# Optimization experiments

Hardware: AMD Instinct MI355X
Metric: run time of the kernel (lower is better)

The kernel has to match this reference:

```python
import jax, jax.numpy as jnp
import numpy as np

P, S, IMG = 8, 4, 256          # patch_size, stride, img_size
HID, GH, B = 64, 128, 4        # conv hidden ch, gcn hidden ch, batch
Ph = (IMG - P) // S + 1        # 63 patches per side
N = Ph * Ph                    # 3969 patch-nodes


def _conv(x, w, b):
    y = jax.lax.conv_general_dilated(x, w, (1, 1), 'SAME',
                                     dimension_numbers=('NCHW', 'OIHW', 'NCHW'))
    return y + b[None, :, None, None]


def _img2patch(x):
    # x: [B,1,H,W] -> [B, N, P*P] (row-major patch pixels, matching torch reshape)
    pt = jax.lax.conv_general_dilated_patches(x, (P, P), (S, S), 'VALID')  # [B, P*P, Ph, Pw]
    b = x.shape[0]
    return pt.reshape(b, P * P, N).transpose(0, 2, 1)


def _patch2img(y):
    # y: [b, N, P*P] -> [b, 1, IMG, IMG] via overlap scatter-add
    b = y.shape[0]
    y = y.reshape(b, Ph, Ph, P, P)
    x = jnp.zeros((b, 1, IMG, IMG), y.dtype)
    hi = S * (Ph - 1) + 1
    for i in range(P):          # fixed small loop over patch pixels (64 iters)
        for j in range(P):
            x = x.at[:, 0, i:i + hi:S, j:j + hi:S].add(y[:, :, :, i, j])
    return x


def _gcn(x, adj, w, bias):
    # x: [B,N,F_in], adj: [B,N,N] -> [B,N,F_out]
    support = jnp.einsum('bnf,fg->bng', x, w)
    return jnp.einsum('bnm,bmg->bng', adj, support) + bias


def setup_inputs() -> dict:
    key = jax.random.key(0)
    ks = jax.random.split(key, 14)
    sc = 0.05
    return {
        'input_data': jax.random.normal(ks[0], (B, 1, IMG, IMG), jnp.float32),
        'proj': jax.random.normal(ks[1], (B, 1, IMG, IMG), jnp.float32),
        'adj': jax.random.uniform(ks[2], (B, N, N), jnp.float32) / N,
        'lam': jnp.float32(0.5),
        'conv_w1': jax.random.normal(ks[3], (HID, 1, 3, 3), jnp.float32) * sc,
        'conv_b1': jnp.zeros((HID,), jnp.float32),
        'conv_w2': jax.random.normal(ks[4], (HID, HID, 3, 3), jnp.float32) * sc,
        'conv_b2': jnp.zeros((HID,), jnp.float32),
        'conv_w3': jax.random.normal(ks[5], (1, HID, 3, 3), jnp.float32) * sc,
        'conv_b3': jnp.zeros((1,), jnp.float32),
        'gcn_w3': jax.random.normal(ks[6], (P * P, GH), jnp.float32) * sc,
        'gcn_b3': jnp.zeros((GH,), jnp.float32),
        'gcn_w4': jax.random.normal(ks[7], (GH, P * P), jnp.float32) * sc,
        'gcn_b4': jnp.zeros((P * P,), jnp.float32),
    }


def reference(input_data, proj, adj, lam,
              conv_w1, conv_b1, conv_w2, conv_b2, conv_w3, conv_b3,
              gcn_w3, gcn_b3, gcn_w4, gcn_b4):
    # block1: data-fidelity step (fidelity_module modeled as DC update)
    tmp1 = input_data + lam * (proj - input_data)
    # block2: 3-layer CNN
    h = jax.nn.relu(_conv(input_data, conv_w1, conv_b1))
    h = jax.nn.relu(_conv(h, conv_w2, conv_b2))
    tmp2 = _conv(h, conv_w3, conv_b3)
    # block3/4: patch-graph GCN branch
    patch = _img2patch(input_data)                 # [B, N, P*P]
    g = jax.nn.relu(_gcn(patch, adj, gcn_w3, gcn_b3))
    g = _gcn(g, adj, gcn_w4, gcn_b4)               # [B, N, P*P]
    # Patch2Im with overlap-count normalization mask
    mask = _patch2img(jnp.ones((1, N, P * P), jnp.float32))
    tmp3 = _patch2img(g) / mask
    return jax.nn.relu(tmp1 + tmp2 + tmp3)
```

## Files before the change

kernel.cpp:

```cpp
#include <hip/hip_runtime.h>

#define IMG   256
#define NPIX  65536
#define PH    63
#define NNODE 3969
#define SN    4000
#define HID   64
#define GH    128
#define BATCH 4

typedef __attribute__((ext_vector_type(8))) short short8;
typedef __attribute__((ext_vector_type(4))) float float4v;
typedef unsigned short ushort_t;

__device__ inline ushort_t f2bf(float f) {
    union { float f; unsigned u; } v; v.f = f;
    unsigned r = v.u + 0x7FFF + ((v.u >> 16) & 1);
    return (ushort_t)(r >> 16);
}

__global__ __launch_bounds__(256) void k_cvt_adj(const float* __restrict__ adj,
                                                 ushort_t* __restrict__ adjb) {
    int n = blockIdx.x, b = blockIdx.y;
    const float* src = adj + (size_t)(b * NNODE + n) * NNODE;
    unsigned* dst = (unsigned*)(adjb + (size_t)(b * NNODE + n) * SN);
    for (int c2 = threadIdx.x; c2 < SN / 2; c2 += 256) {
        int c = c2 * 2;
        float f0 = (c < NNODE) ? src[c] : 0.f;
        float f1 = (c + 1 < NNODE) ? src[c + 1] : 0.f;
        dst[c2] = (unsigned)f2bf(f0) | ((unsigned)f2bf(f1) << 16);
    }
}

__global__ __launch_bounds__(256) void k_sup1(const float* __restrict__ in,
                                              const float* __restrict__ w3,
                                              ushort_t* __restrict__ sup1T) {
    int b = blockIdx.z;
    int g = blockIdx.y * 8 + (threadIdx.x >> 5);
    int n = blockIdx.x * 32 + (threadIdx.x & 31);
    ushort_t* dst = sup1T + (size_t)b * GH * SN + (size_t)g * SN + n;
    if (n >= NNODE) { *dst = 0; return; }
    int py = n / PH, px = n - py * PH;
    const float* base = in + (size_t)b * NPIX + (py * 4) * IMG + px * 4;
    float acc = 0.f;
#pragma unroll
    for (int i = 0; i < 8; ++i) {
        float4v v0 = *(const float4v*)&base[i * IMG];
        float4v v1 = *(const float4v*)&base[i * IMG + 4];
        const float* wrow = w3 + (i * 8) * GH + g;
#pragma unroll
        for (int j = 0; j < 4; ++j) acc += v0[j] * wrow[j * GH];
#pragma unroll
        for (int j = 0; j < 4; ++j) acc += v1[j] * wrow[(4 + j) * GH];
    }
    *dst = f2bf(acc);
}

template <int G>
__global__ __launch_bounds__(256) void k_gemm_mfma(const ushort_t* __restrict__ adjb,
                                                   const ushort_t* __restrict__ supT,
                                                   float* __restrict__ C) {
    constexpr int FN = (G == 128) ? 4 : 2;
    const int b = blockIdx.z, ks = blockIdx.y;
    const int node0 = blockIdx.x * 128;
    const int t = threadIdx.x;
    const int lane = t & 63, w = t >> 6;
    const int l15 = lane & 15, q = lane >> 4;
    const int wm0 = (G == 128) ? (w & 1) * 64 : 0;
    const int wn0 = (G == 128) ? (w >> 1) * 64 : w * 32;

    __shared__ ushort_t Als[G][72];
    __shared__ ushort_t Bls[128][72];

    const int k0c = ks * 512;
    const int kend = (k0c + 512 < NNODE) ? (k0c + 512) : NNODE;
    const int kiters = (kend - k0c + 31) >> 5;
    const int npairs = (kiters + 1) >> 1;

    const ushort_t* Ab = supT + (size_t)b * G * SN;
    const ushort_t* Bb = adjb + (size_t)b * NNODE * SN;
    float* Cb = C + (size_t)b * G * SN;

    float4v acc[4][FN];
#pragma unroll
    for (int i = 0; i < 4; ++i)
#pragma unroll
        for (int j = 0; j < FN; ++j)
#pragma unroll
            for (int r = 0; r < 4; ++r) acc[i][j][r] = 0.f;

    for (int kp = 0; kp < npairs; ++kp) {
        const int kb0 = k0c + kp * 64;
        const bool has2 = (kp * 2 + 1 < kiters);
#pragma unroll
        for (int i = 0; i < G / 64; ++i) {
            int idx = t + i * 256;
            int r = idx >> 2, s = idx & 3;
            *(uint4*)&Als[r][s * 8] =
                *(const uint4*)&Ab[(size_t)r * SN + kb0 + s * 8];
        }
#pragma unroll
        for (int i = 0; i < 2; ++i) {
            int idx = t + i * 256;
            int r = idx >> 2, s = idx & 3;
            *(uint4*)&Bls[r][s * 8] =
                *(const uint4*)&Bb[(size_t)(node0 + r) * SN + kb0 + s * 8];
        }
        if (has2) {
#pragma unroll
            for (int i = 0; i < G / 64; ++i) {
                int idx = t + i * 256;
                int r = idx >> 2, s = idx & 3;
                *(uint4*)&Als[r][32 + s * 8] =
                    *(const uint4*)&Ab[(size_t)r * SN + kb0 + 32 + s * 8];
            }
#pragma unroll
            for (int i = 0; i < 2; ++i) {
                int idx = t + i * 256;
                int r = idx >> 2, s = idx & 3;
                *(uint4*)&Bls[r][32 + s * 8] =
                    *(const uint4*)&Bb[(size_t)(node0 + r) * SN + kb0 + 32 + s * 8];
            }
        }
        __syncthreads();
        {
            short8 af[4], bf[FN];
#pragma unroll
            for (int i = 0; i < 4; ++i)
                af[i] = *(const short8*)&Als[wm0 + i * 16 + l15][q * 8];
#pragma unroll
            for (int j = 0; j < FN; ++j)
                bf[j] = *(const short8*)&Bls[wn0 + j * 16 + l15][q * 8];
#pragma unroll
            for (int i = 0; i < 4; ++i)
#pragma unroll
                for (int j = 0; j < FN; ++j)
                    acc[i][j] = __builtin_amdgcn_mfma_f32_16x16x32_bf16(
                        af[i], bf[j], acc[i][j], 0, 0, 0);
        }
        if (has2) {
            short8 af[4], bf[FN];
#pragma unroll
            for (int i = 0; i < 4; ++i)
                af[i] = *(const short8*)&Als[wm0 + i * 16 + l15][32 + q * 8];
#pragma unroll
            for (int j = 0; j < FN; ++j)
                bf[j] = *(const short8*)&Bls[wn0 + j * 16 + l15][32 + q * 8];
#pragma unroll
            for (int i = 0; i < 4; ++i)
#pragma unroll
                for (int j = 0; j < FN; ++j)
                    acc[i][j] = __builtin_amdgcn_mfma_f32_16x16x32_bf16(
                        af[i], bf[j], acc[i][j], 0, 0, 0);
        }
        __syncthreads();
    }
#pragma unroll
    for (int i = 0; i < 4; ++i) {
        int gg = wm0 + i * 16 + q * 4;
#pragma unroll
        for (int j = 0; j < FN; ++j) {
            int nn = node0 + wn0 + j * 16 + l15;
            if (nn < NNODE) {
#pragma unroll
                for (int r = 0; r < 4; ++r)
                    unsafeAtomicAdd(&Cb[(size_t)(gg + r) * SN + nn], acc[i][j][r]);
            }
        }
    }
}

__global__ __launch_bounds__(256) void k_sup2(const float* __restrict__ g1T,
                                              const float* __restrict__ gb3,
                                              const float* __restrict__ w4,
                                              ushort_t* __restrict__ sup2T) {
    int b = blockIdx.z;
    int g = blockIdx.y * 8 + (threadIdx.x >> 5);
    int n = blockIdx.x * 32 + (threadIdx.x & 31);
    const float* gb = g1T + (size_t)b * GH * SN + n;
    float acc = 0.f;
#pragma unroll 8
    for (int k = 0; k < GH; ++k) {
        float v = fmaxf(gb[(size_t)k * SN] + gb3[k], 0.f);
        acc += v * w4[k * 64 + g];
    }
    sup2T[(size_t)b * 64 * SN + (size_t)g * SN + n] = (n < NNODE) ? f2bf(acc) : 0;
}

__global__ __launch_bounds__(256) void k_prepack(const float* __restrict__ w,
                                                 ushort_t* __restrict__ W2p) {
    int idx = blockIdx.x * 256 + threadIdx.x;
    if (idx >= 36864) return;
    int tap = idx >> 12, rem = idx & 4095;
    int oc = rem >> 6, ic = rem & 63;
    W2p[idx] = f2bf(w[(oc * 64 + ic) * 9 + tap]);
}

__global__ __launch_bounds__(256) void k_conv2f(const float* __restrict__ in,
                                                const float* __restrict__ w1,
                                                const float* __restrict__ b1,
                                                const ushort_t* __restrict__ W2p,
                                                const float* __restrict__ b2,
                                                const float* __restrict__ w3c,
                                                float* __restrict__ U) {
    __shared__ ushort_t Xs[340 * 72];
    __shared__ float pre[1088];
    const int b = blockIdx.z;
    const float* inb = in + (size_t)b * NPIX;
    float* Uball = U + (size_t)b * 9 * NPIX;
    const int t = threadIdx.x;
    const int lane = t & 63, w = t >> 6;
    const int l15 = lane & 15, q = lane >> 4;
    const int x0 = blockIdx.x * 32, y0 = blockIdx.y * 8;

    float* sI  = pre;
    float* ws1 = pre + 432;
    float* bs1 = pre + 1008;

    for (int idx = t; idx < 432; idx += 256) {
        int yy = idx / 36, xx = idx - yy * 36;
        int gy = y0 + yy - 2, gx = x0 + xx - 2;
        sI[idx] = (gy >= 0 && gy < IMG && gx >= 0 && gx < IMG) ? inb[gy * IMG + gx] : 0.f;
    }
    for (int idx = t; idx < 576; idx += 256) ws1[idx] = w1[idx];
    if (t < 64) bs1[t] = b1[t];
    __syncthreads();

    for (int idx = t; idx < 2720; idx += 256) {
        int hp = idx >> 3, s = idx & 7;
        int hy = hp / 34, hx = hp - hy * 34;
        int gy = y0 + hy - 1, gx = x0 + hx - 1;
        unsigned pk[4] = {0u, 0u, 0u, 0u};
        if (gy >= 0 && gy < IMG && gx >= 0 && gx < IMG) {
            float r[9];
#pragma unroll
            for (int dy = 0; dy < 3; ++dy)
#pragma unroll
                for (int dx = 0; dx < 3; ++dx)
                    r[dy * 3 + dx] = sI[(hy + dy) * 36 + hx + dx];
#pragma unroll
            for (int h = 0; h < 4; ++h) {
                int oc0 = s * 8 + h * 2;
                float a0 = bs1[oc0], a1 = bs1[oc0 + 1];
#pragma unroll
                for (int k = 0; k < 9; ++k) {
                    a0 += r[k] * ws1[oc0 * 9 + k];
                    a1 += r[k] * ws1[(oc0 + 1) * 9 + k];
                }
                a0 = fmaxf(a0, 0.f); a1 = fmaxf(a1, 0.f);
                pk[h] = (unsigned)f2bf(a0) | ((unsigned)f2bf(a1) << 16);
            }
        }
        *(uint4*)&Xs[hp * 72 + s * 8] = *(uint4*)pk;
    }
    __syncthreads();

    for (int idx = t; idx < 576; idx += 256) pre[idx] = w3c[idx];

    const int wn0 = w * 64;
    int pbase[4];
#pragma unroll
    for (int j = 0; j < 4; ++j) {
        int p = wn0 + j * 16 + l15;
        pbase[j] = (p >> 5) * 34 + (p & 31);
    }

    float4v acc[4][4];
#pragma unroll
    for (int i = 0; i < 4; ++i)
#pragma unroll
        for (int j = 0; j < 4; ++j)
#pragma unroll
            for (int r = 0; r < 4; ++r) acc[i][j][r] = 0.f;

    for (int tap = 0; tap < 9; ++tap) {
        int ky = tap / 3, kx = tap - ky * 3;
        const ushort_t* wp = W2p + tap * 4096;
#pragma unroll
        for (int c = 0; c < 2; ++c) {
            short8 af[4], bf[4];
#pragma unroll
            for (int i = 0; i < 4; ++i)
                af[i] = *(const short8*)&wp[(i * 16 + l15) * 64 + c * 32 + q * 8];
#pragma unroll
            for (int j = 0; j < 4; ++j)
                bf[j] = *(const short8*)&Xs[(pbase[j] + ky * 34 + kx) * 72 + c * 32 + q * 8];
#pragma unroll
            for (int i = 0; i < 4; ++i)
#pragma unroll
                for (int j = 0; j < 4; ++j)
                    acc[i][j] = __builtin_amdgcn_mfma_f32_16x16x32_bf16(
                        af[i], bf[j], acc[i][j], 0, 0, 0);
        }
    }
    __syncthreads();

    float b2r[16];
#pragma unroll
    for (int i = 0; i < 4; ++i)
#pragma unroll
        for (int r = 0; r < 4; ++r) b2r[i * 4 + r] = b2[i * 16 + q * 4 + r];

#pragma unroll
    for (int j = 0; j < 4; ++j) {
        float u[9];
#pragma unroll
        for (int d = 0; d < 9; ++d) u[d] = 0.f;
#pragma unroll
        for (int i = 0; i < 4; ++i)
#pragma unroll
            for (int r = 0; r < 4; ++r) {
                int oc = i * 16 + q * 4 + r;
                float h = fmaxf(acc[i][j][r] + b2r[i * 4 + r], 0.f);
#pragma unroll
                for (int d = 0; d < 9; ++d) u[d] += h * pre[oc * 9 + d];
            }
#pragma unroll
        for (int d = 0; d < 9; ++d) {
            u[d] += __shfl_xor(u[d], 16, 64);
            u[d] += __shfl_xor(u[d], 32, 64);
        }
        int p = wn0 + j * 16 + l15;
        int y = y0 + (p >> 5), x = x0 + (p & 31);
#pragma unroll
        for (int dd = 0; dd < 3; ++dd) {
            int d = q + dd * 4;
            if (d < 9)
                Uball[(size_t)d * NPIX + (size_t)y * IMG + x] = u[d];
        }
    }
}

__global__ __launch_bounds__(256) void k_combine(const float* __restrict__ in,
                                                 const float* __restrict__ proj,
                                                 const float* __restrict__ lamp,
                                                 const float* __restrict__ U,
                                                 const float* __restrict__ bc,
                                                 const float* __restrict__ g2T,
                                                 const float* __restrict__ gb4,
                                                 float* __restrict__ out) {
    int b = blockIdx.z;
    const float* inb = in + (size_t)b * NPIX;
    const float* prb = proj + (size_t)b * NPIX;
    const float* Ub = U + (size_t)b * 9 * NPIX;
    const float* g2b = g2T + (size_t)b * 64 * SN;
    int tx = threadIdx.x & 15, ty = threadIdx.x >> 4;
    int x = blockIdx.x * 16 + tx, y = blockIdx.y * 16 + ty;

    float acc = bc[0];
#pragma unroll
    for (int dy = 0; dy < 3; ++dy) {
        int yy = y + dy - 1;
#pragma unroll
        for (int dx = 0; dx < 3; ++dx) {
            int xx = x + dx - 1;
            if (yy >= 0 && yy < IMG && xx >= 0 && xx < IMG)
                acc += Ub[(size_t)(dy * 3 + dx) * NPIX + (size_t)yy * IMG + xx];
        }
    }

    float iv = inb[y * IMG + x], pv = prb[y * IMG + x];
    float tmp1 = iv + lamp[0] * (pv - iv);

    int pylo = (y >= 4) ? ((y - 4) >> 2) : 0;
    int pyhi = min(62, y >> 2);
    int pxlo = (x >= 4) ? ((x - 4) >> 2) : 0;
    int pxhi = min(62, x >> 2);
    float sum = 0.f;
    int cnt = 0;
    for (int py = pylo; py <= pyhi; ++py)
        for (int px = pxlo; px <= pxhi; ++px) {
            int pix = (y - 4 * py) * 8 + (x - 4 * px);
            sum += g2b[(size_t)pix * SN + (py * PH + px)] + gb4[pix];
            ++cnt;
        }
    float tmp3 = sum / (float)cnt;

    out[(size_t)b * NPIX + y * IMG + x] = fmaxf(tmp1 + acc + tmp3, 0.f);
}

extern "C" void kernel_launch(void* const* d_in, const int* in_sizes, int n_in,
                              void* d_out, int out_size, void* d_ws, size_t ws_size,
                              hipStream_t stream) {
    const float* input = (const float*)d_in[0];
    const float* proj  = (const float*)d_in[1];
    const float* adj   = (const float*)d_in[2];
    const float* lam   = (const float*)d_in[3];
    const float* cw1   = (const float*)d_in[4];
    const float* cb1   = (const float*)d_in[5];
    const float* cw2   = (const float*)d_in[6];
    const float* cb2   = (const float*)d_in[7];
    const float* cw3   = (const float*)d_in[8];
    const float* cb3   = (const float*)d_in[9];
    const float* gw3   = (const float*)d_in[10];
    const float* gb3   = (const float*)d_in[11];
    const float* gw4   = (const float*)d_in[12];
    const float* gb4   = (const float*)d_in[13];
    float* out = (float*)d_out;

    char* base = (char*)d_ws;
    float*    g2T   = (float*)base;
    char*     pool  = base + 4096000;
    ushort_t* adjb  = (ushort_t*)pool;
    ushort_t* sup1T = (ushort_t*)(pool + 127008000);
    float*    g1T   = (float*)(pool + 127008000 + 4096000);
    ushort_t* sup2T = (ushort_t*)(pool + 127008000 + 4096000 + 8192000);
    float*    U     = (float*)pool;
    ushort_t* W2p   = (ushort_t*)(pool + 9437184);

    dim3 blk(256);

    hipMemsetAsync(g1T, 0, 8192000, stream);
    hipMemsetAsync(g2T, 0, 4096000, stream);

    k_cvt_adj<<<dim3(NNODE, BATCH), blk, 0, stream>>>(adj, adjb);
    k_sup1<<<dim3(125, 16, BATCH), blk, 0, stream>>>(input, gw3, sup1T);
    k_gemm_mfma<128><<<dim3(32, 8, BATCH), blk, 0, stream>>>(adjb, sup1T, g1T);
    k_sup2<<<dim3(125, 8, BATCH), blk, 0, stream>>>(g1T, gb3, gw4, sup2T);
    k_gemm_mfma<64><<<dim3(32, 8, BATCH), blk, 0, stream>>>(adjb, sup2T, g2T);

    k_prepack<<<dim3(144), blk, 0, stream>>>(cw2, W2p);
    k_conv2f<<<dim3(8, 32, BATCH), blk, 0, stream>>>(input, cw1, cb1, W2p, cb2, cw3, U);
    k_combine<<<dim3(16, 16, BATCH), blk, 0, stream>>>(
        input, proj, lam, U, cb3, g2T, gb4, out);
}
```

Measured before the change: 694.9 us.

## Replace split-K atomic accumulation with partial buffers and a reduction kernel

The two adjacency GEMMs now split K into 4 chunks instead of 8. Each chunk writes plain stores into its own partial buffer rather than atomically adding into a zeroed output. A small float4 reduction kernel then sums the four partials, and the two memsets are removed. This removes atomic traffic and memset launches but adds extra kernel launches and extra write/read traffic for the partial buffers, and halves the grid's parallelism.

```diff
diff --git a/kernel.cpp b/kernel.cpp
--- a/kernel.cpp
+++ b/kernel.cpp
@@ -59,7 +59,7 @@
 template <int G>
 __global__ __launch_bounds__(256) void k_gemm_mfma(const ushort_t* __restrict__ adjb,
                                                    const ushort_t* __restrict__ supT,
-                                                   float* __restrict__ C) {
+                                                   float* __restrict__ Cp) {
     constexpr int FN = (G == 128) ? 4 : 2;
     const int b = blockIdx.z, ks = blockIdx.y;
     const int node0 = blockIdx.x * 128;
@@ -72,14 +72,14 @@
     __shared__ ushort_t Als[G][72];
     __shared__ ushort_t Bls[128][72];
 
-    const int k0c = ks * 512;
-    const int kend = (k0c + 512 < NNODE) ? (k0c + 512) : NNODE;
+    const int k0c = ks * 992;
+    const int kend = (ks == 3) ? NNODE : k0c + 992;
     const int kiters = (kend - k0c + 31) >> 5;
     const int npairs = (kiters + 1) >> 1;
 
     const ushort_t* Ab = supT + (size_t)b * G * SN;
     const ushort_t* Bb = adjb + (size_t)b * NNODE * SN;
-    float* Cb = C + (size_t)b * G * SN;
+    float* Cb = Cp + (size_t)ks * BATCH * G * SN + (size_t)b * G * SN;
 
     float4v acc[4][FN];
 #pragma unroll
@@ -164,10 +164,25 @@
             if (nn < NNODE) {
 #pragma unroll
                 for (int r = 0; r < 4; ++r)
-                    unsafeAtomicAdd(&Cb[(size_t)(gg + r) * SN + nn], acc[i][j][r]);
+                    Cb[(size_t)(gg + r) * SN + nn] = acc[i][j][r];
             }
         }
     }
+}
+
+__global__ __launch_bounds__(256) void k_red4(const float* __restrict__ in,
+                                              float* __restrict__ out,
+                                              int n4, int q4) {
+    int i = blockIdx.x * 256 + threadIdx.x;
+    if (i >= n4) return;
+    const float4v* in4 = (const float4v*)in;
+    float4v a = in4[i];
+    float4v b = in4[i + q4];
+    float4v c = in4[i + 2 * q4];
+    float4v d = in4[i + 3 * q4];
+#pragma unroll
+    for (int r = 0; r < 4; ++r) a[r] = (a[r] + b[r]) + (c[r] + d[r]);
+    ((float4v*)out)[i] = a;
 }
 
 __global__ __launch_bounds__(256) void k_sup2(const float* __restrict__ g1T,
@@ -403,21 +418,23 @@
     char*     pool  = base + 4096000;
     ushort_t* adjb  = (ushort_t*)pool;
     ushort_t* sup1T = (ushort_t*)(pool + 127008000);
-    float*    g1T   = (float*)(pool + 127008000 + 4096000);
-    ushort_t* sup2T = (ushort_t*)(pool + 127008000 + 4096000 + 8192000);
-    float*    U     = (float*)pool;
-    ushort_t* W2p   = (ushort_t*)(pool + 9437184);
+    float*    g1T   = (float*)(pool + 131104000);
+    ushort_t* sup2T = (ushort_t*)(pool + 139296000);
+    char*     shared = pool + 141344000;
+    float*    g1P   = (float*)shared;
+    float*    g2P   = (float*)shared;
+    float*    U     = (float*)shared;
+    ushort_t* W2p   = (ushort_t*)(shared + 9437184);
 
     dim3 blk(256);
-
-    hipMemsetAsync(g1T, 0, 8192000, stream);
-    hipMemsetAsync(g2T, 0, 4096000, stream);
 
     k_cvt_adj<<<dim3(NNODE, BATCH), blk, 0, stream>>>(adj, adjb);
     k_sup1<<<dim3(125, 16, BATCH), blk, 0, stream>>>(input, gw3, sup1T);
-    k_gemm_mfma<128><<<dim3(32, 8, BATCH), blk, 0, stream>>>(adjb, sup1T, g1T);
+    k_gemm_mfma<128><<<dim3(32, 4, BATCH), blk, 0, stream>>>(adjb, sup1T, g1P);
+    k_red4<<<dim3(2000), blk, 0, stream>>>(g1P, g1T, 512000, 512000);
     k_sup2<<<dim3(125, 8, BATCH), blk, 0, stream>>>(g1T, gb3, gw4, sup2T);
-    k_gemm_mfma<64><<<dim3(32, 8, BATCH), blk, 0, stream>>>(adjb, sup2T, g2T);
+    k_gemm_mfma<64><<<dim3(32, 4, BATCH), blk, 0, stream>>>(adjb, sup2T, g2P);
+    k_red4<<<dim3(1000), blk, 0, stream>>>(g2P, g2T, 256000, 256000);
 
     k_prepack<<<dim3(144), blk, 0, stream>>>(cw2, W2p);
     k_conv2f<<<dim3(8, 32, BATCH), blk, 0, stream>>>(input, cw1, cb1, W2p, cb2, cw3, U);
```

New measurement: 659.0 us. 5.2% less time.
